# Performance work log

Hardware: AMD Instinct MI355X
Metric: run time of the kernel (lower is better)

Reference implementation:

```python
import jax, jax.numpy as jnp
import numpy as np

B, H, N, D, HID, NIT = 8, 16, 2048, 64, 256, 4
LR = 1.0


def setup_inputs() -> dict:
    key = jax.random.key(0)
    kq, kk, kv, k1, k2 = jax.random.split(key, 5)
    q = jax.random.normal(kq, (B, H, N, D), jnp.float32)
    k = jax.random.normal(kk, (B, H, N, D), jnp.float32)
    v = jax.random.normal(kv, (B, H, N, D), jnp.float32)
    # xavier_uniform per-head init for the 2-layer inner encoder
    l1 = float(np.sqrt(6.0 / (D + HID)))
    l2 = float(np.sqrt(6.0 / (HID + D)))
    W1 = jax.random.uniform(k1, (H, D, HID), jnp.float32, -l1, l1)
    W2 = jax.random.uniform(k2, (H, HID, D), jnp.float32, -l2, l2)
    return {"q": q, "k": k, "v": v, "W1": W1, "W2": W2, "training": 1, "return_aux": 0}


def _enc(params, x):
    # per-head 2-layer MLP: x (H, M, D) -> (H, M, D); no bias, no LN, no residual
    W1, W2 = params
    h = jax.nn.gelu(jnp.einsum('hmd,hde->hme', x, W1))  # flax nn.gelu = approximate gelu
    return jnp.einsum('hme,heo->hmo', h, W2)


def _inner_loss(params, data):
    x = data[..., :D]
    y = data[..., D:]
    return 0.5 * jnp.mean(jnp.square(y - _enc(params, x))) * H


def reference(q, k, v, W1, W2, training, return_aux):
    ilr = jnp.ones((NIT, H), jnp.float32) * LR
    # train set: inputs=k, targets=v (no inp/trg LN, no trg_proj with out_dim=None)
    data = jnp.concatenate([k, v], axis=-1)  # (B, H, N, 2D)
    chunk = N // NIT
    # split along N into NIT mini-batches, stacked on a scan axis: (B, NIT, H, chunk, 2D)
    data = data.reshape(B, H, NIT, chunk, 2 * D).transpose(0, 2, 1, 3, 4)

    def step(params, ilr_data):
        lr, d = ilr_data  # lr: (H,), d: (H, chunk, 2D)
        _, grads = jax.value_and_grad(_inner_loss)(params, d)
        params = jax.tree_util.tree_map(
            lambda p, g: p - lr.reshape(-1, 1, 1) * g, params, grads)
        return params, None

    # learnable_init=False -> stop_gradient on initial inner params
    init = (jax.lax.stop_gradient(W1), jax.lax.stop_gradient(W2))

    def inner_loop(db):  # db: (NIT, H, chunk, 2D)
        final, _ = jax.lax.scan(step, init, (ilr, db))
        return final

    final_params = jax.vmap(inner_loop)(data)  # leaves have leading B
    test_out = jax.vmap(_enc)(final_params, q)  # (B, H, N, D)
    return test_out.transpose(0, 2, 1, 3).reshape(B, N, H * D)
```

## Files before the change

### kernel.cpp

```cpp
#include <hip/hip_runtime.h>
#include <hip/hip_bf16.h>

typedef __hip_bfloat16 bf16;
typedef __attribute__((ext_vector_type(8))) short frag8;
typedef __attribute__((ext_vector_type(4))) float frag4f;
typedef __attribute__((ext_vector_type(4))) short short4v;

#define BB 8
#define HH 16
#define NTOK 2048
#define DD 64
#define HID 256
#define NIT 4
#define CH 512
#define NP 128
#define INV_CD 3.0517578125e-05f

#define MFMA(a,b,c) __builtin_amdgcn_mfma_f32_16x16x32_bf16((a),(b),(c),0,0,0)

#define SW(row,col) ((col) ^ ((((row)>>3)&3)<<4))

__device__ __forceinline__ short f2b(float f){
    union { __hip_bfloat16 b; short s; } u;
    u.b = __float2bfloat16(f);
    return u.s;
}

__device__ __forceinline__ float tanh_fast(float u){
    float e = __expf(2.0f*u);
    return 1.0f - 2.0f/(e+1.0f);
}

__device__ __forceinline__ float gelu_f(float x){
    const float c0 = 0.7978845608028654f, c1 = 0.044715f;
    float u = c0*(x + c1*x*x*x);
    float t = tanh_fast(u);
    return 0.5f*x*(1.0f+t);
}

__device__ __forceinline__ void gelu_both(float x, float* hv, float* gp){
    const float c0 = 0.7978845608028654f, c1 = 0.044715f;
    float x2 = x*x;
    float u = c0*(x + c1*x2*x);
    float t = tanh_fast(u);
    *hv = 0.5f*x*(1.0f+t);
    *gp = 0.5f*(1.0f+t) + 0.5f*x*(1.0f-t*t)*c0*(1.0f+3.0f*c1*x2);
}

__global__ __launch_bounds__(1024, 4) void k_step(
    const float* __restrict__ kin, const float* __restrict__ vin,
    const float* __restrict__ MoW1, const float* __restrict__ MoW2,
    const float* __restrict__ Pin,  float* __restrict__ Mnew,
    float* __restrict__ Pout, int hIdx, int fold, int t)
{
    int p = blockIdx.x >> 1, half = blockIdx.x & 1;
    int tid = threadIdx.x;
    int w = tid >> 6, lane = tid & 63, q = lane >> 4, ln = lane & 15;
    int s = w >> 2, ch = w & 3;

    __shared__ __attribute__((aligned(16))) short W1c[256*72];
    __shared__ __attribute__((aligned(16))) short W2c[64*264];
    __shared__ __attribute__((aligned(16))) short hl [64*264];
    __shared__ __attribute__((aligned(16))) short el [64*72];
    __shared__ __attribute__((aligned(16))) short eTl[64*72];
    __shared__ __attribute__((aligned(16))) short dzTl[256*72];

    {
        int widx = hIdx ? (p & 15) : p;
        const float* w1o = MoW1 + (size_t)widx*16384;
        const float* w2o = MoW2 + (size_t)widx*16384;
        const float* pa = Pin + (size_t)p*32768;
        const float* pb = Pin + (size_t)(NP+p)*32768;
        float* mn1 = Mnew + (size_t)p*16384;
        float* mn2 = Mnew + (size_t)(NP+p)*16384;
        #pragma unroll 4
        for (int i=0;i<16;i++){
            int src = i*1024 + tid;
            float a = w1o[src];
            float b = w2o[src];
            if (fold){
                a -= pa[src] + pb[src];
                b -= pa[16384+src] + pb[16384+src];
            }
            mn1[src] = a;
            mn2[src] = b;
            W1c[(src & 255)*72  + (src >> 8)] = f2b(a);
            W2c[(src & 63)*264  + SW(src & 63, src >> 6)] = f2b(b);
        }
    }
    __syncthreads();

    frag4f dw1[4], dw2[4];
    #pragma unroll
    for (int i=0;i<4;i++){ frag4f zz = {0.f,0.f,0.f,0.f}; dw1[i]=zz; dw2[i]=zz; }

    size_t rowbase = (size_t)p*NTOK + (size_t)t*CH + (size_t)half*256;

    #pragma unroll 1
    for (int mt=0; mt<4; ++mt){
        int m0 = mt*64;

        frag8 af[2];
        {
            const float* xb = kin + (rowbase + m0 + s*16 + ln)*DD;
            #pragma unroll
            for (int kk=0;kk<2;kk++){
                const float* xr = xb + kk*32 + q*8;
                float4 u0 = *(const float4*)xr;
                float4 u1 = *(const float4*)(xr+4);
                frag8 a;
                a[0]=f2b(u0.x); a[1]=f2b(u0.y); a[2]=f2b(u0.z); a[3]=f2b(u0.w);
                a[4]=f2b(u1.x); a[5]=f2b(u1.y); a[6]=f2b(u1.z); a[7]=f2b(u1.w);
                af[kk]=a;
            }
        }
        frag4f zacc[4];
        #pragma unroll
        for (int nti=0;nti<4;nti++){
            frag4f zc = {0.f,0.f,0.f,0.f};
            #pragma unroll
            for (int kk=0;kk<2;kk++){
                frag8 b = *(const frag8*)&W1c[((ch*4+nti)*16+ln)*72 + kk*32 + q*8];
                zc = MFMA(af[kk], b, zc);
            }
            zacc[nti] = zc;
        }
        #pragma unroll
        for (int nti=0;nti<4;nti++)
            #pragma unroll
            for (int r=0;r<4;r++){
                float hv, gp;
                gelu_both(zacc[nti][r], &hv, &gp);
                int row = s*16+q*4+r;
                hl[row*264 + SW(row, (ch*4+nti)*16 + ln)] = f2b(hv);
                zacc[nti][r] = gp;
            }
        __syncthreads();

        {
            frag8 hfr[8];
            #pragma unroll
            for (int kk=0;kk<8;kk++)
                hfr[kk] = *(const frag8*)&hl[(s*16+ln)*264 + SW(s*16+ln, kk*32 + q*8)];
            frag4f oc = {0.f,0.f,0.f,0.f};
            #pragma unroll
            for (int kk=0;kk<8;kk++){
                frag8 b = *(const frag8*)&W2c[(ch*16+ln)*264 + SW(ch*16+ln, kk*32 + q*8)];
                oc = MFMA(hfr[kk], b, oc);
            }
            short4v ep;
            #pragma unroll
            for (int r=0;r<4;r++){
                float y = vin[(rowbase + m0 + s*16 + q*4 + r)*DD + ch*16 + ln];
                float e = (oc[r]-y)*INV_CD;
                el[(s*16+q*4+r)*72 + ch*16 + ln] = f2b(e);
                ep[r] = f2b(e);
            }
            *(short4v*)&eTl[(ch*16+ln)*72 + s*16 + q*4] = ep;
        }
        __syncthreads();

        {
            frag8 efr[2];
            #pragma unroll
            for (int kk=0;kk<2;kk++)
                efr[kk] = *(const frag8*)&el[(s*16+ln)*72 + kk*32 + q*8];
            #pragma unroll
            for (int nti=0;nti<4;nti++){
                int nt = ch*4 + nti;
                frag4f dc = {0.f,0.f,0.f,0.f};
                #pragma unroll
                for (int kk=0;kk<2;kk++){
                    frag8 b;
                    #pragma unroll
                    for (int j=0;j<8;j++){
                        int row = kk*32+q*8+j;
                        b[j] = W2c[row*264 + SW(row, nt*16 + ln)];
                    }
                    dc = MFMA(efr[kk], b, dc);
                }
                short4v dp;
                #pragma unroll
                for (int r=0;r<4;r++)
                    dp[r] = f2b(dc[r]*zacc[nti][r]);
                *(short4v*)&dzTl[(nt*16+ln)*72 + s*16 + q*4] = dp;
            }
        }
        __syncthreads();

        {
            #pragma unroll
            for (int kk2=0;kk2<2;kk2++){
                frag8 a;
                #pragma unroll
                for (int j=0;j<8;j++)
                    a[j] = f2b(kin[(rowbase + m0 + kk2*32 + q*8 + j)*DD + s*16 + ln]);
                #pragma unroll
                for (int nti=0;nti<4;nti++){
                    frag8 b = *(const frag8*)&dzTl[((ch*4+nti)*16+ln)*72 + kk2*32 + q*8];
                    dw1[nti] = MFMA(a, b, dw1[nti]);
                }
            }
            #pragma unroll
            for (int kk2=0;kk2<2;kk2++){
                frag8 a;
                #pragma unroll
                for (int j=0;j<8;j++){
                    int row = kk2*32+q*8+j;
                    a[j] = hl[row*264 + SW(row, w*16 + ln)];
                }
                #pragma unroll
                for (int ot=0;ot<4;ot++){
                    frag8 b = *(const frag8*)&eTl[(ot*16+ln)*72 + kk2*32 + q*8];
                    dw2[ot] = MFMA(a, b, dw2[ot]);
                }
            }
        }
        __syncthreads();
    }

    {
        float* pw1 = Pout + ((size_t)half*NP + p)*32768;
        float* pw2 = pw1 + 16384;
        #pragma unroll
        for (int nti=0;nti<4;nti++)
            #pragma unroll
            for (int r=0;r<4;r++)
                pw1[(s*16 + q*4 + r)*256 + (ch*4+nti)*16 + ln] = dw1[nti][r];
        #pragma unroll
        for (int ot=0;ot<4;ot++)
            #pragma unroll
            for (int r=0;r<4;r++)
                pw2[(w*16 + q*4 + r)*64 + ot*16 + ln] = dw2[ot][r];
    }
}

__global__ __launch_bounds__(256) void k_castW(const float* __restrict__ M0,
                                               const float* __restrict__ P1,
                                               short* __restrict__ W1p,
                                               short* __restrict__ W2p){
    int g = blockIdx.x*256 + threadIdx.x;
    int lane = g & 63;
    int slot = (g >> 6) & 63;
    int p = g / (64*64);
    int q = lane >> 4, ln = lane & 15;
    const float* m1 = M0 + (size_t)p*16384;
    const float* m2 = M0 + (size_t)(NP+p)*16384;
    const float* pa = P1 + (size_t)p*32768;
    const float* pb = P1 + (size_t)(NP+p)*32768;
    if (slot < 32){
        int nt = slot >> 1, kk = slot & 1;
        short* dst = W1p + (((size_t)p*32 + slot)*64 + lane)*8;
        #pragma unroll
        for (int j=0;j<8;j++){
            int idx = (kk*32 + q*8 + j)*HID + nt*16 + ln;
            dst[j] = f2b(m1[idx] - pa[idx] - pb[idx]);
        }
    } else {
        int s2 = slot - 32;
        int nt = s2 >> 3, kk = s2 & 7;
        short* dst = W2p + (((size_t)p*32 + s2)*64 + lane)*8;
        #pragma unroll
        for (int j=0;j<8;j++){
            int idx = (kk*32 + q*8 + j)*DD + nt*16 + ln;
            dst[j] = f2b(m2[idx] - pa[16384+idx] - pb[16384+idx]);
        }
    }
}

__global__ __launch_bounds__(256) void k_apply(const float* __restrict__ qin,
                                               const short* __restrict__ W1p,
                                               const short* __restrict__ W2p,
                                               float* __restrict__ out){
    int p = blockIdx.x >> 5, mt = blockIdx.x & 31;
    int tid = threadIdx.x;
    int w = tid >> 6, lane = tid & 63, q = lane >> 4, ln = lane & 15;
    int m0 = mt*64;
    int b = p >> 4, h = p & 15;
    __shared__ __attribute__((aligned(16))) short hl[64*264];
    float* ol = (float*)hl;
    const float* xbase = qin + ((size_t)p*NTOK + m0 + w*16 + ln)*DD;
    frag8 af[2];
    #pragma unroll
    for (int kk=0;kk<2;kk++){
        const float* xr = xbase + kk*32 + q*8;
        float4 u0 = *(const float4*)xr;
        float4 u1 = *(const float4*)(xr+4);
        frag8 a;
        a[0]=f2b(u0.x); a[1]=f2b(u0.y); a[2]=f2b(u0.z); a[3]=f2b(u0.w);
        a[4]=f2b(u1.x); a[5]=f2b(u1.y); a[6]=f2b(u1.z); a[7]=f2b(u1.w);
        af[kk]=a;
    }
    const short* w1b = W1p + ((size_t)p*32*64 + lane)*8;
    #pragma unroll
    for (int nt=0;nt<16;nt++){
        frag4f zc = {0.f,0.f,0.f,0.f};
        #pragma unroll
        for (int kk=0;kk<2;kk++){
            frag8 bfr = *(const frag8*)(w1b + (size_t)(nt*2+kk)*64*8);
            zc = MFMA(af[kk], bfr, zc);
        }
        #pragma unroll
        for (int r=0;r<4;r++){
            int row = w*16 + q*4 + r;
            hl[row*264 + SW(row, nt*16 + ln)] = f2b(gelu_f(zc[r]));
        }
    }
    __syncthreads();
    frag8 hfr[8];
    #pragma unroll
    for (int kk=0;kk<8;kk++)
        hfr[kk] = *(const frag8*)(&hl[(w*16+ln)*264 + SW(w*16+ln, kk*32 + q*8)]);
    __syncthreads();
    const short* w2b = W2p + ((size_t)p*32*64 + lane)*8;
    frag4f oc4[4];
    #pragma unroll
    for (int nt=0;nt<4;nt++){
        frag4f oc = {0.f,0.f,0.f,0.f};
        #pragma unroll
        for (int kk=0;kk<8;kk++){
            frag8 bfr = *(const frag8*)(w2b + (size_t)(nt*8+kk)*64*8);
            oc = MFMA(hfr[kk], bfr, oc);
        }
        oc4[nt] = oc;
    }
    #pragma unroll
    for (int nt=0;nt<4;nt++)
        #pragma unroll
        for (int r=0;r<4;r++)
            ol[(w*16+q*4+r)*68 + nt*16 + ln] = oc4[nt][r];
    __syncthreads();
    size_t obase = ((size_t)b*NTOK + m0)*(HH*DD) + (size_t)h*DD;
    int c8 = tid & 7;
    #pragma unroll
    for (int pass=0; pass<2; pass++){
        int row = pass*32 + (tid>>3);
        #pragma unroll
        for (int u=0; u<2; u++){
            float4 vv = *(const float4*)&ol[row*68 + (c8 + u*8)*4];
            *(float4*)&out[obase + (size_t)row*(HH*DD) + (c8 + u*8)*4] = vv;
        }
    }
}

extern "C" void kernel_launch(void* const* d_in, const int* in_sizes, int n_in,
                              void* d_out, int out_size, void* d_ws, size_t ws_size,
                              hipStream_t stream) {
    (void)in_sizes; (void)n_in; (void)out_size; (void)ws_size;
    const float* q  = (const float*)d_in[0];
    const float* k  = (const float*)d_in[1];
    const float* v  = (const float*)d_in[2];
    const float* W1 = (const float*)d_in[3];
    const float* W2 = (const float*)d_in[4];
    float* out = (float*)d_out;

    float* P0  = (float*)d_ws;
    short* W1p = (short*)d_ws;
    short* W2p = W1p + (size_t)NP*16384;

    float* M0 = (float*)d_out;
    float* M1 = M0 + (size_t)NP*32768;
    float* P1 = M1 + (size_t)NP*32768;

    k_step<<<256,1024,0,stream>>>(k, v,  W1,   W2,                        P0,  M1,  P0,  1,   0,  0);
    k_step<<<256,1024,0,stream>>>(k, v,  M1,   M1+(size_t)NP*16384,       P0,  M0,  P1,  0,   1,  1);
    k_step<<<256,1024,0,stream>>>(k, v,  M0,   M0+(size_t)NP*16384,       P1,  M1,  P0,  0,   1,  2);
    k_step<<<256,1024,0,stream>>>(k, v,  M1,   M1+(size_t)NP*16384,       P0,  M0,  P1,  0,   1,  3);
    k_castW<<<NP*16, 256, 0, stream>>>(M0, P1, W1p, W2p);
    k_apply<<<NP*32, 256, 0, stream>>>(q, W1p, W2p, out);
}
```

Before: 504.6 us.

## Coalesce weight cast through LDS, dedupe master writes, transpose first MFMA in apply

In k_step, only the half==0 block now writes the updated fp32 master weights, so the second block no longer stores a duplicate copy. k_castW now runs one 1024-thread block per head and matrix: it reads the master weights and partial gradients with coalesced float4 loads into padded LDS, then emits packed bf16 fragments as vector stores, replacing scattered strided global reads. In k_apply, the first MFMA swaps its operands so each lane holds four consecutive hidden columns, which lets it write gelu outputs as one short4 store without the swizzle. All three target memory-access efficiency in small kernels around the main step loop.

```diff
diff --git a/kernel.cpp b/kernel.cpp
--- a/kernel.cpp
+++ b/kernel.cpp
@@ -82,8 +82,10 @@
                 a -= pa[src] + pb[src];
                 b -= pa[16384+src] + pb[16384+src];
             }
-            mn1[src] = a;
-            mn2[src] = b;
+            if (half == 0){
+                mn1[src] = a;
+                mn2[src] = b;
+            }
             W1c[(src & 255)*72  + (src >> 8)] = f2b(a);
             W2c[(src & 63)*264  + SW(src & 63, src >> 6)] = f2b(b);
         }
@@ -235,35 +237,54 @@
     }
 }
 
-__global__ __launch_bounds__(256) void k_castW(const float* __restrict__ M0,
-                                               const float* __restrict__ P1,
-                                               short* __restrict__ W1p,
-                                               short* __restrict__ W2p){
-    int g = blockIdx.x*256 + threadIdx.x;
-    int lane = g & 63;
-    int slot = (g >> 6) & 63;
-    int p = g / (64*64);
-    int q = lane >> 4, ln = lane & 15;
-    const float* m1 = M0 + (size_t)p*16384;
-    const float* m2 = M0 + (size_t)(NP+p)*16384;
-    const float* pa = P1 + (size_t)p*32768;
-    const float* pb = P1 + (size_t)(NP+p)*32768;
-    if (slot < 32){
-        int nt = slot >> 1, kk = slot & 1;
-        short* dst = W1p + (((size_t)p*32 + slot)*64 + lane)*8;
-        #pragma unroll
-        for (int j=0;j<8;j++){
-            int idx = (kk*32 + q*8 + j)*HID + nt*16 + ln;
-            dst[j] = f2b(m1[idx] - pa[idx] - pb[idx]);
-        }
-    } else {
-        int s2 = slot - 32;
-        int nt = s2 >> 3, kk = s2 & 7;
-        short* dst = W2p + (((size_t)p*32 + s2)*64 + lane)*8;
-        #pragma unroll
-        for (int j=0;j<8;j++){
-            int idx = (kk*32 + q*8 + j)*DD + nt*16 + ln;
-            dst[j] = f2b(m2[idx] - pa[16384+idx] - pb[16384+idx]);
+__global__ __launch_bounds__(1024) void k_castW(const float* __restrict__ M0,
+                                                const float* __restrict__ P1,
+                                                short* __restrict__ W1p,
+                                                short* __restrict__ W2p){
+    int p = blockIdx.x >> 1, which = blockIdx.x & 1;
+    int tid = threadIdx.x;
+    __shared__ float F[256*65];
+    const float* m  = M0 + ((size_t)(which ? NP+p : p))*16384;
+    const float* pa = P1 + (size_t)p*32768      + (size_t)which*16384;
+    const float* pb = P1 + (size_t)(NP+p)*32768 + (size_t)which*16384;
+
+    #pragma unroll
+    for (int i=0;i<4;i++){
+        int idx4 = i*4096 + tid*4;
+        float4 mv = *(const float4*)(m  + idx4);
+        float4 av = *(const float4*)(pa + idx4);
+        float4 bv = *(const float4*)(pb + idx4);
+        float vv[4] = { mv.x-av.x-bv.x, mv.y-av.y-bv.y, mv.z-av.z-bv.z, mv.w-av.w-bv.w };
+        if (which == 0){
+            int row = idx4 >> 8, col = idx4 & 255;
+            #pragma unroll
+            for (int e=0;e<4;e++) F[row*257 + col + e] = vv[e];
+        } else {
+            int row = idx4 >> 6, col = idx4 & 63;
+            #pragma unroll
+            for (int e=0;e<4;e++) F[row*65 + col + e] = vv[e];
+        }
+    }
+    __syncthreads();
+
+    #pragma unroll
+    for (int inst=0;inst<2;inst++){
+        int fi = inst*1024 + tid;
+        int slot = fi >> 6, l = fi & 63;
+        int qf = l >> 4, lnf = l & 15;
+        frag8 v;
+        if (which == 0){
+            int nt = slot >> 1, kk = slot & 1;
+            #pragma unroll
+            for (int j=0;j<8;j++)
+                v[j] = f2b(F[(kk*32 + qf*8 + j)*257 + nt*16 + lnf]);
+            *(frag8*)(W1p + (((size_t)p*32 + slot)*64 + l)*8) = v;
+        } else {
+            int nt = slot >> 3, kk = slot & 7;
+            #pragma unroll
+            for (int j=0;j<8;j++)
+                v[j] = f2b(F[(kk*32 + qf*8 + j)*65 + nt*16 + lnf]);
+            *(frag8*)(W2p + (((size_t)p*32 + slot)*64 + l)*8) = v;
         }
     }
 }
@@ -298,19 +319,19 @@
         #pragma unroll
         for (int kk=0;kk<2;kk++){
             frag8 bfr = *(const frag8*)(w1b + (size_t)(nt*2+kk)*64*8);
-            zc = MFMA(af[kk], bfr, zc);
-        }
-        #pragma unroll
-        for (int r=0;r<4;r++){
-            int row = w*16 + q*4 + r;
-            hl[row*264 + SW(row, nt*16 + ln)] = f2b(gelu_f(zc[r]));
-        }
+            zc = MFMA(bfr, af[kk], zc);
+        }
+        short4v hp;
+        #pragma unroll
+        for (int r=0;r<4;r++)
+            hp[r] = f2b(gelu_f(zc[r]));
+        *(short4v*)&hl[(w*16+ln)*264 + nt*16 + q*4] = hp;
     }
     __syncthreads();
     frag8 hfr[8];
     #pragma unroll
     for (int kk=0;kk<8;kk++)
-        hfr[kk] = *(const frag8*)(&hl[(w*16+ln)*264 + SW(w*16+ln, kk*32 + q*8)]);
+        hfr[kk] = *(const frag8*)(&hl[(w*16+ln)*264 + kk*32 + q*8]);
     __syncthreads();
     const short* w2b = W2p + ((size_t)p*32*64 + lane)*8;
     frag4f oc4[4];
@@ -366,6 +387,6 @@
     k_step<<<256,1024,0,stream>>>(k, v,  M1,   M1+(size_t)NP*16384,       P0,  M0,  P1,  0,   1,  1);
     k_step<<<256,1024,0,stream>>>(k, v,  M0,   M0+(size_t)NP*16384,       P1,  M1,  P0,  0,   1,  2);
     k_step<<<256,1024,0,stream>>>(k, v,  M1,   M1+(size_t)NP*16384,       P0,  M0,  P1,  0,   1,  3);
-    k_castW<<<NP*16, 256, 0, stream>>>(M0, P1, W1p, W2p);
+    k_castW<<<NP*2, 1024, 0, stream>>>(M0, P1, W1p, W2p);
     k_apply<<<NP*32, 256, 0, stream>>>(q, W1p, W2p, out);
 }
```

Result: no change. 500.5 us (-0.8%).
